# Optimization experiments

Hardware: AMD Instinct MI355X
Metric: run time of the kernel (lower is better)

Reference implementation:

```python
import jax, jax.numpy as jnp
import numpy as np

N_EMBD = 1024
N_HEAD = 16
HEAD_DIM = N_EMBD // N_HEAD
SEQ = 2048
BATCH = 2
WINDOW = 256
SCALE = 1.0 / np.sqrt(HEAD_DIM)
MASK_VALUE = -10000.0


def setup_inputs() -> dict:
    key = jax.random.key(0)
    ks = jax.random.split(key, 5)
    s = 0.02
    return {
        "hidden_states": jax.random.normal(ks[0], (BATCH, SEQ, N_EMBD), dtype=jnp.float32),
        "w_attn": jax.random.normal(ks[1], (N_EMBD, 3 * N_EMBD), dtype=jnp.float32) * s,
        "b_attn": jnp.zeros((3 * N_EMBD,), dtype=jnp.float32),
        "w_proj": jax.random.normal(ks[2], (N_EMBD, N_EMBD), dtype=jnp.float32) * s,
        "b_proj": jnp.zeros((N_EMBD,), dtype=jnp.float32),
    }


def _mask(seq_len):
    # causal AND sliding window: j <= i and j > i - WINDOW
    i = jnp.arange(seq_len)[:, None]
    j = jnp.arange(seq_len)[None, :]
    return (j <= i) & (j > i - WINDOW)  # [T, T] bool


def reference(hidden_states, w_attn, b_attn, w_proj, b_proj):
    B, T, _ = hidden_states.shape
    qkv = hidden_states @ w_attn + b_attn  # [B, T, 3E]
    q, k, v = jnp.split(qkv, 3, axis=-1)
    # [B, H, T, D]
    q = q.reshape(B, T, N_HEAD, HEAD_DIM).transpose(0, 2, 1, 3)
    k = k.reshape(B, T, N_HEAD, HEAD_DIM).transpose(0, 2, 1, 3)
    v = v.reshape(B, T, N_HEAD, HEAD_DIM).transpose(0, 2, 1, 3)

    scores = jnp.einsum("bhqd,bhkd->bhqk", q, k) * SCALE  # [B, H, T, T]
    mask = _mask(T)[None, None]  # [1, 1, T, T]
    scores = jnp.where(mask, scores, MASK_VALUE)
    scores = jnp.clip(scores, -10000.0, 10000.0)
    attn = jax.nn.softmax(scores, axis=-1)
    out = jnp.einsum("bhqk,bhkd->bhqd", attn, v)  # [B, H, T, D]
    out = out.transpose(0, 2, 1, 3).reshape(B, T, N_EMBD)
    return out @ w_proj + b_proj
```

## Files before the change

kernel.cpp:

```cpp
#include <hip/hip_runtime.h>


typedef __bf16 bf16_t;
typedef bf16_t bf16x8 __attribute__((ext_vector_type(8)));
typedef bf16_t bf16x4 __attribute__((ext_vector_type(4)));
typedef float  floatx4 __attribute__((ext_vector_type(4)));

#define SEQ_T   2048
#define NHEAD   16
#define HDIM    64
#define EMB     1024
#define WIN     256
#define SCALE_F 0.125f

__global__ __launch_bounds__(1024) void detect_dtype(
    const uint4* __restrict__ w, int nvec, int* __restrict__ flag)
{
    __shared__ int cnt_s;
    if (threadIdx.x == 0) cnt_s = 0;
    __syncthreads();
    int c = 0;
    for (int i = threadIdx.x; i < nvec; i += 1024) {
        const uint4 v = w[i];
        #pragma unroll
        for (int e = 0; e < 4; ++e) {
            const unsigned int word = (&v.x)[e];
            const unsigned int ex = (word >> 7) & 0xffu;
            c += (ex >= 100u && ex <= 150u) ? 1 : 0;
        }
    }
    #pragma unroll
    for (int m = 32; m >= 1; m >>= 1) c += __shfl_xor(c, m, 64);
    if ((threadIdx.x & 63) == 0) atomicAdd(&cnt_s, c);
    __syncthreads();
    if (threadIdx.x == 0) *flag = (cnt_s * 2 > nvec * 4) ? 1 : 0;
}

__global__ __launch_bounds__(256) void canon_bf16(
    const void* __restrict__ src, bf16_t* __restrict__ dst, int n,
    const int* __restrict__ flag)
{
    const int f = *flag;
    const int i4 = (blockIdx.x * 256 + threadIdx.x) * 4;
    if (i4 >= n) return;
    bf16x4 v;
    if (f) {
        v = *(const bf16x4*)((const bf16_t*)src + i4);
    } else {
        const float4 x = *(const float4*)((const float*)src + i4);
        v[0] = (bf16_t)x.x; v[1] = (bf16_t)x.y;
        v[2] = (bf16_t)x.z; v[3] = (bf16_t)x.w;
    }
    *(bf16x4*)(dst + i4) = v;
}

__global__ __launch_bounds__(256) void transpose_to_bf16(
    const void* __restrict__ W, bf16_t* __restrict__ Wt, int K, int N,
    const int* __restrict__ flag)
{
    __shared__ __align__(16) bf16_t tile[64][68];
    const int f  = *flag;
    const int n0 = blockIdx.x * 64;
    const int k0 = blockIdx.y * 64;
    const int tx = threadIdx.x & 15;
    const int ty = threadIdx.x >> 4;

    #pragma unroll
    for (int r = ty; r < 64; r += 16) {
        bf16x4 v;
        const size_t base = (size_t)(k0 + r) * N + n0 + tx * 4;
        if (f) {
            v = *(const bf16x4*)((const bf16_t*)W + base);
        } else {
            const float4 x = *(const float4*)((const float*)W + base);
            v[0] = (bf16_t)x.x; v[1] = (bf16_t)x.y;
            v[2] = (bf16_t)x.z; v[3] = (bf16_t)x.w;
        }
        *(bf16x4*)&tile[r][tx * 4] = v;
    }
    __syncthreads();
    #pragma unroll
    for (int r = ty; r < 64; r += 16) {
        bf16x4 v;
        v[0] = tile[tx * 4 + 0][r];
        v[1] = tile[tx * 4 + 1][r];
        v[2] = tile[tx * 4 + 2][r];
        v[3] = tile[tx * 4 + 3][r];
        *(bf16x4*)(Wt + (size_t)(n0 + r) * K + k0 + tx * 4) = v;
    }
}

template<int BNt>
__global__ __launch_bounds__(256) void gemm_bt_bias(
    const bf16_t* __restrict__ A,
    const bf16_t* __restrict__ Bt,
    const bf16_t* __restrict__ bias,
    void* __restrict__ C,
    int M, int N, int K,
    int force_bf16, const int* __restrict__ flag)
{
    constexpr int BMt = 128;
    constexpr int NF  = BNt / 32;
    __shared__ __align__(16) bf16_t As[BMt * 64];
    __shared__ __align__(16) bf16_t Bs[BNt * 64];

    const int obf  = force_bf16 | *flag;
    const int tid  = threadIdx.x;
    const int wave = tid >> 6;
    const int lane = tid & 63;
    const int quad = lane >> 4;
    const int n16  = lane & 15;
    const int m0 = blockIdx.y * BMt;
    const int n0 = blockIdx.x * BNt;
    const int wm = (wave >> 1) * 64;
    const int wn = (wave & 1) * (BNt / 2);

    floatx4 acc[4][NF] = {};

    const int lr = lane >> 3;
    const int g8 = ((lane & 7) ^ lr) * 8;

    const int csw = (quad ^ (n16 & 7)) * 8;

    for (int k0 = 0; k0 < K; k0 += 64) {
        #pragma unroll
        for (int t = 0; t < BMt / 32; ++t) {
            const int row0 = wave * (BMt / 4) + t * 8;
            const bf16_t* ga = A + (size_t)(m0 + row0 + lr) * K + k0 + g8;
            __builtin_amdgcn_global_load_lds(
                (const __attribute__((address_space(1))) void*)ga,
                (__attribute__((address_space(3))) void*)(As + row0 * 64),
                16, 0, 0);
        }
        #pragma unroll
        for (int t = 0; t < BNt / 32; ++t) {
            const int row0 = wave * (BNt / 4) + t * 8;
            const bf16_t* gb = Bt + (size_t)(n0 + row0 + lr) * K + k0 + g8;
            __builtin_amdgcn_global_load_lds(
                (const __attribute__((address_space(1))) void*)gb,
                (__attribute__((address_space(3))) void*)(Bs + row0 * 64),
                16, 0, 0);
        }
        __syncthreads();

        #pragma unroll
        for (int s = 0; s < 2; ++s) {
            const int ch = (((4 * s + quad) ^ (n16 & 7)) * 8);
            const bf16_t* pa = As + (wm + n16) * 64 + ch;
            const bf16_t* pb = Bs + (wn + n16) * 64 + ch;
            bf16x8 af[4], bfr[NF];
            #pragma unroll
            for (int ff = 0; ff < 4; ++ff)
                af[ff] = *(const bf16x8*)(pa + ff * 16 * 64);
            #pragma unroll
            for (int ff = 0; ff < NF; ++ff)
                bfr[ff] = *(const bf16x8*)(pb + ff * 16 * 64);
            #pragma unroll
            for (int mf = 0; mf < 4; ++mf)
                #pragma unroll
                for (int nf = 0; nf < NF; ++nf)
                    acc[mf][nf] = __builtin_amdgcn_mfma_f32_16x16x32_bf16(
                        af[mf], bfr[nf], acc[mf][nf], 0, 0, 0);
        }
        __syncthreads();
    }

    const int col   = n0 + wn + n16;
    const int rbase = m0 + wm + quad * 4;
    #pragma unroll
    for (int nf = 0; nf < NF; ++nf) {
        const float bv = (float)bias[col + nf * 16];
        #pragma unroll
        for (int mf = 0; mf < 4; ++mf) {
            #pragma unroll
            for (int r = 0; r < 4; ++r) {
                const size_t idx =
                    (size_t)(rbase + mf * 16 + r) * N + col + nf * 16;
                const float val = acc[mf][nf][r] + bv;
                if (obf) ((bf16_t*)C)[idx] = (bf16_t)val;
                else     ((float*)C)[idx]  = val;
            }
        }
    }
}

#define CW   160
#define VT_S 168
#define P_S  168

__global__ __launch_bounds__(256) void attn_mfma(
    const bf16_t* __restrict__ qkv,
    bf16_t* __restrict__ attn_out)
{
    __shared__ __align__(16) bf16_t Ks[CW * 64];
    __shared__ __align__(16) bf16_t Vt[64 * VT_S];
    __shared__ __align__(16) bf16_t Pst[4][16 * P_S];

    const int tid  = threadIdx.x;
    const int wave = tid >> 6;
    const int lane = tid & 63;
    const int quad = lane >> 4;
    const int n16  = lane & 15;

    const int i0 = blockIdx.x * 64;
    const int h  = blockIdx.y;
    const int b  = blockIdx.z;
    const size_t rowbase = (size_t)b * SEQ_T;
    const int kbase  = i0 - 256;
    const int iw     = 16 * wave;
    const int climit = 256 - i0;

    const bf16_t* Qg = qkv + (rowbase + i0 + iw + n16) * (3 * EMB) + h * HDIM;
    bf16x8 qf[2];
    qf[0] = *(const bf16x8*)(Qg + quad * 8);
    qf[1] = *(const bf16x8*)(Qg + 32 + quad * 8);

    floatx4 Oac[4] = {};
    float m_run[4], l_run[4];
    #pragma unroll
    for (int rr = 0; rr < 4; ++rr) { m_run[rr] = -3.0e38f; l_run[rr] = 0.f; }

    for (int hc = 0; hc < 2; ++hc) {
        const int cbase = hc * CW;

        bf16x8 vreg[5];
        #pragma unroll
        for (int t = 0; t < 5; ++t) {
            const int idx = tid + 256 * t;
            const int lc  = idx >> 3;
            const int d0  = (idx & 7) * 8;
            int j = kbase + cbase + lc; if (j < 0) j = 0;
            vreg[t] = *(const bf16x8*)(qkv + (rowbase + j) * (3 * EMB)
                                       + 2 * EMB + h * HDIM + d0);
        }

        __syncthreads();

        #pragma unroll
        for (int t = 0; t < 5; ++t) {
            const int lc0 = wave * 40 + t * 8;
            const int lcL = lc0 + (lane >> 3);
            int j = kbase + cbase + lcL; if (j < 0) j = 0;
            const int g = (lane & 7) ^ (lcL & 7);
            const bf16_t* src = qkv + (rowbase + j) * (3 * EMB)
                                + EMB + h * HDIM + g * 8;
            __builtin_amdgcn_global_load_lds(
                (const __attribute__((address_space(1))) void*)src,
                (__attribute__((address_space(3))) void*)(Ks + lc0 * 64),
                16, 0, 0);
        }

        #pragma unroll
        for (int t = 0; t < 5; ++t) {
            const int idx = tid + 256 * t;
            const int lc  = idx >> 3;
            const int d0  = (idx & 7) * 8;
            #pragma unroll
            for (int e = 0; e < 8; ++e)
                Vt[(d0 + e) * VT_S + lc] = vreg[t][e];
        }

        __syncthreads();

        floatx4 sc[10];
        #pragma unroll
        for (int tt = 0; tt < 10; ++tt) {
            sc[tt] = (floatx4){0.f, 0.f, 0.f, 0.f};
            #pragma unroll
            for (int s2 = 0; s2 < 2; ++s2) {
                const int lc = 16 * tt + n16;
                const int ch = (4 * s2 + quad) ^ (lc & 7);
                const bf16x8 kf = *(const bf16x8*)(Ks + lc * 64 + ch * 8);
                sc[tt] = __builtin_amdgcn_mfma_f32_16x16x32_bf16(
                    qf[s2], kf, sc[tt], 0, 0, 0);
            }
        }

        #pragma unroll
        for (int tt = 0; tt < 10; ++tt) {
            const int c  = cbase + 16 * tt + n16;
            const int cw = c - iw;
            #pragma unroll
            for (int rr = 0; rr < 4; ++rr) {
                const int r = quad * 4 + rr;
                const bool valid = (cw > r) && (cw <= r + 256) && (c >= climit);
                sc[tt][rr] = valid ? sc[tt][rr] * SCALE_F : -3.0e38f;
            }
        }

        float cm[4];
        #pragma unroll
        for (int rr = 0; rr < 4; ++rr) {
            cm[rr] = -3.0e38f;
            #pragma unroll
            for (int tt = 0; tt < 10; ++tt) cm[rr] = fmaxf(cm[rr], sc[tt][rr]);
            #pragma unroll
            for (int m = 8; m >= 1; m >>= 1)
                cm[rr] = fmaxf(cm[rr], __shfl_xor(cm[rr], m, 64));
        }

        #pragma unroll
        for (int rr = 0; rr < 4; ++rr) {
            const float mnew  = fmaxf(m_run[rr], cm[rr]);
            const float alpha = __expf(m_run[rr] - mnew);
            m_run[rr] = mnew;
            l_run[rr] *= alpha;
            #pragma unroll
            for (int nt = 0; nt < 4; ++nt) Oac[nt][rr] *= alpha;
        }

        float psum[4] = {0.f, 0.f, 0.f, 0.f};
        #pragma unroll
        for (int tt = 0; tt < 10; ++tt) {
            #pragma unroll
            for (int rr = 0; rr < 4; ++rr) {
                const float s = sc[tt][rr];
                const float e = (s > -1.0e38f) ? __expf(s - m_run[rr]) : 0.f;
                psum[rr] += e;
                Pst[wave][(quad * 4 + rr) * P_S + 16 * tt + n16] = (bf16_t)e;
            }
        }
        #pragma unroll
        for (int rr = 0; rr < 4; ++rr) {
            #pragma unroll
            for (int m = 8; m >= 1; m >>= 1)
                psum[rr] += __shfl_xor(psum[rr], m, 64);
            l_run[rr] += psum[rr];
        }

        __syncthreads();

        #pragma unroll
        for (int ks = 0; ks < 5; ++ks) {
            const bf16x8 paf = *(const bf16x8*)(
                &Pst[wave][n16 * P_S + ks * 32 + quad * 8]);
            #pragma unroll
            for (int nt = 0; nt < 4; ++nt) {
                const bf16x8 vbf = *(const bf16x8*)(
                    Vt + (nt * 16 + n16) * VT_S + ks * 32 + quad * 8);
                Oac[nt] = __builtin_amdgcn_mfma_f32_16x16x32_bf16(
                    paf, vbf, Oac[nt], 0, 0, 0);
            }
        }
    }

    #pragma unroll
    for (int rr = 0; rr < 4; ++rr) {
        const float rden = 1.0f / l_run[rr];
        const size_t row = rowbase + i0 + iw + quad * 4 + rr;
        #pragma unroll
        for (int nt = 0; nt < 4; ++nt) {
            attn_out[row * EMB + h * HDIM + nt * 16 + n16] =
                (bf16_t)(Oac[nt][rr] * rden);
        }
    }
}

extern "C" void kernel_launch(void* const* d_in, const int* in_sizes, int n_in,
                              void* d_out, int out_size, void* d_ws, size_t ws_size,
                              hipStream_t stream)
{
    const void* hidden = d_in[0];
    const void* w_attn = d_in[1];
    const void* b_attn = d_in[2];
    const void* w_proj = d_in[3];
    const void* b_proj = d_in[4];

    char* ws = (char*)d_ws;
    bf16_t* Wt_attn = (bf16_t*)(ws);
    bf16_t* Wt_proj = (bf16_t*)(ws + (6u << 20));
    bf16_t* qkv     = (bf16_t*)(ws + (8u << 20));
    bf16_t* attn_o  = (bf16_t*)(ws + (32u << 20));
    bf16_t* Hc      = (bf16_t*)(ws + (40u << 20));
    bf16_t* bb_attn = (bf16_t*)(ws + (48u << 20));
    bf16_t* bb_proj = (bf16_t*)(ws + (48u << 20) + 8192);
    int*    flag    = (int*)   (ws + (48u << 20) + 16384);

    detect_dtype<<<1, 1024, 0, stream>>>((const uint4*)hidden, 4096, flag);

    canon_bf16<<<4096, 256, 0, stream>>>(hidden, Hc, 4096 * 1024, flag);
    canon_bf16<<<3, 256, 0, stream>>>(b_attn, bb_attn, 3072, flag);
    canon_bf16<<<1, 256, 0, stream>>>(b_proj, bb_proj, 1024, flag);

    transpose_to_bf16<<<dim3(3072 / 64, 1024 / 64), 256, 0, stream>>>(
        w_attn, Wt_attn, 1024, 3072, flag);
    transpose_to_bf16<<<dim3(1024 / 64, 1024 / 64), 256, 0, stream>>>(
        w_proj, Wt_proj, 1024, 1024, flag);

    gemm_bt_bias<128><<<dim3(3072 / 128, 4096 / 128), 256, 0, stream>>>(
        Hc, Wt_attn, bb_attn, qkv, 4096, 3072, 1024, 1, flag);

    attn_mfma<<<dim3(SEQ_T / 64, NHEAD, 2), 256, 0, stream>>>(qkv, attn_o);

    gemm_bt_bias<64><<<dim3(1024 / 64, 4096 / 128), 256, 0, stream>>>(
        attn_o, Wt_proj, bb_proj, (void*)d_out, 4096, 1024, 1024, 0, flag);
}
```

Baseline: 190.9 us.

## Fuse preprocessing launches, inline dtype detection, register-staged GEMM prefetch

The separate dtype-detect kernel is replaced by a per-wave inline check of the first 64 vectors of the input. The three canonicalisation launches become one, and the two weight transposes become one, which cuts launch count. When inputs are already bf16 the conversion is skipped and the GEMM reads the raw buffers. The GEMM drops direct global-to-LDS loads in favour of a register-staged prefetch of the next K tile with a swizzled LDS store. This may overlap loads with MFMA work, but it adds register pressure and loses the async LDS load path.

```diff
diff --git a/kernel.cpp b/kernel.cpp
--- a/kernel.cpp
+++ b/kernel.cpp
@@ -13,55 +13,56 @@
 #define WIN     256
 #define SCALE_F 0.125f
 
-__global__ __launch_bounds__(1024) void detect_dtype(
-    const uint4* __restrict__ w, int nvec, int* __restrict__ flag)
-{
-    __shared__ int cnt_s;
-    if (threadIdx.x == 0) cnt_s = 0;
-    __syncthreads();
+__device__ __forceinline__ int detect_bf16(const uint4* __restrict__ det)
+{
+    const int lane = threadIdx.x & 63;
+    const uint4 v = det[lane];
     int c = 0;
-    for (int i = threadIdx.x; i < nvec; i += 1024) {
-        const uint4 v = w[i];
-        #pragma unroll
-        for (int e = 0; e < 4; ++e) {
-            const unsigned int word = (&v.x)[e];
-            const unsigned int ex = (word >> 7) & 0xffu;
-            c += (ex >= 100u && ex <= 150u) ? 1 : 0;
-        }
+    #pragma unroll
+    for (int e = 0; e < 4; ++e) {
+        const unsigned int ex = ((&v.x)[e] >> 7) & 0xffu;
+        c += (ex >= 100u && ex <= 150u) ? 1 : 0;
     }
     #pragma unroll
     for (int m = 32; m >= 1; m >>= 1) c += __shfl_xor(c, m, 64);
-    if ((threadIdx.x & 63) == 0) atomicAdd(&cnt_s, c);
-    __syncthreads();
-    if (threadIdx.x == 0) *flag = (cnt_s * 2 > nvec * 4) ? 1 : 0;
-}
-
-__global__ __launch_bounds__(256) void canon_bf16(
-    const void* __restrict__ src, bf16_t* __restrict__ dst, int n,
-    const int* __restrict__ flag)
-{
-    const int f = *flag;
-    const int i4 = (blockIdx.x * 256 + threadIdx.x) * 4;
-    if (i4 >= n) return;
+    return (c * 2 > 256) ? 1 : 0;
+}
+
+__global__ __launch_bounds__(256) void canon_all(
+    const void* __restrict__ hidden, bf16_t* __restrict__ Hc,
+    const void* __restrict__ ba, bf16_t* __restrict__ bba,
+    const void* __restrict__ bp, bf16_t* __restrict__ bbp)
+{
+    if (detect_bf16((const uint4*)hidden)) return;
+    const int blk = blockIdx.x;
+    const float* src;
+    bf16_t* dst;
+    int base;
+    if (blk < 4096)      { src = (const float*)hidden; dst = Hc;  base = blk * 1024; }
+    else if (blk < 4099) { src = (const float*)ba;     dst = bba; base = (blk - 4096) * 1024; }
+    else                 { src = (const float*)bp;     dst = bbp; base = 0; }
+    const int i4 = base + threadIdx.x * 4;
+    const float4 x = *(const float4*)(src + i4);
     bf16x4 v;
-    if (f) {
-        v = *(const bf16x4*)((const bf16_t*)src + i4);
-    } else {
-        const float4 x = *(const float4*)((const float*)src + i4);
-        v[0] = (bf16_t)x.x; v[1] = (bf16_t)x.y;
-        v[2] = (bf16_t)x.z; v[3] = (bf16_t)x.w;
-    }
+    v[0] = (bf16_t)x.x; v[1] = (bf16_t)x.y;
+    v[2] = (bf16_t)x.z; v[3] = (bf16_t)x.w;
     *(bf16x4*)(dst + i4) = v;
 }
 
-__global__ __launch_bounds__(256) void transpose_to_bf16(
-    const void* __restrict__ W, bf16_t* __restrict__ Wt, int K, int N,
-    const int* __restrict__ flag)
+__global__ __launch_bounds__(256) void transpose_both(
+    const void* __restrict__ wA, bf16_t* __restrict__ WtA,
+    const void* __restrict__ wP, bf16_t* __restrict__ WtP,
+    const uint4* __restrict__ det)
 {
     __shared__ __align__(16) bf16_t tile[64][68];
-    const int f  = *flag;
-    const int n0 = blockIdx.x * 64;
-    const int k0 = blockIdx.y * 64;
+    const int f = detect_bf16(det);
+    int id = blockIdx.x;
+    const void* W; bf16_t* Wt; int N, bx, by;
+    if (id < 768) { W = wA; Wt = WtA; N = 3072; bx = id % 48; by = id / 48; }
+    else { id -= 768; W = wP; Wt = WtP; N = 1024; bx = id % 16; by = id / 16; }
+    const int K = 1024;
+    const int n0 = bx * 64;
+    const int k0 = by * 64;
     const int tx = threadIdx.x & 15;
     const int ty = threadIdx.x >> 4;
 
@@ -92,19 +93,26 @@
 
 template<int BNt>
 __global__ __launch_bounds__(256) void gemm_bt_bias(
-    const bf16_t* __restrict__ A,
+    const bf16_t* __restrict__ Abf,
+    const bf16_t* __restrict__ Aalt,
     const bf16_t* __restrict__ Bt,
-    const bf16_t* __restrict__ bias,
+    const bf16_t* __restrict__ biasbf,
+    const bf16_t* __restrict__ biasalt,
     void* __restrict__ C,
     int M, int N, int K,
-    int force_bf16, const int* __restrict__ flag)
+    int force_bf16, const uint4* __restrict__ det)
 {
     constexpr int BMt = 128;
     constexpr int NF  = BNt / 32;
+    constexpr int NB  = BNt / 32;
     __shared__ __align__(16) bf16_t As[BMt * 64];
     __shared__ __align__(16) bf16_t Bs[BNt * 64];
 
-    const int obf  = force_bf16 | *flag;
+    const int flag = detect_bf16(det);
+    const bf16_t* A    = flag ? Abf    : Aalt;
+    const bf16_t* bias = flag ? biasbf : biasalt;
+    const int obf = force_bf16 | flag;
+
     const int tid  = threadIdx.x;
     const int wave = tid >> 6;
     const int lane = tid & 63;
@@ -117,30 +125,46 @@
 
     floatx4 acc[4][NF] = {};
 
-    const int lr = lane >> 3;
-    const int g8 = ((lane & 7) ^ lr) * 8;
-
-    const int csw = (quad ^ (n16 & 7)) * 8;
+    uint4 rA[4], rB[NB];
+
+    const int arow = tid >> 1;
+    const int acol = (tid & 1) * 32;
+    const int brow = (BNt == 128) ? (tid >> 1) : (tid >> 2);
+    const int bcol = (BNt == 128) ? ((tid & 1) * 32) : ((tid & 3) * 16);
+
+    auto loadA = [&](int kk) {
+        const bf16_t* g = A + (size_t)(m0 + arow) * K + kk + acol;
+        #pragma unroll
+        for (int i = 0; i < 4; ++i) rA[i] = *(const uint4*)(g + i * 8);
+    };
+    auto loadB = [&](int kk) {
+        const bf16_t* g = Bt + (size_t)(n0 + brow) * K + kk + bcol;
+        #pragma unroll
+        for (int i = 0; i < NB; ++i) rB[i] = *(const uint4*)(g + i * 8);
+    };
+    auto storeA = [&]() {
+        #pragma unroll
+        for (int i = 0; i < 4; ++i) {
+            const int g = (acol >> 3) + i;
+            const int s = g ^ (arow & 7);
+            *(uint4*)(As + arow * 64 + s * 8) = rA[i];
+        }
+    };
+    auto storeB = [&]() {
+        #pragma unroll
+        for (int i = 0; i < NB; ++i) {
+            const int g = (bcol >> 3) + i;
+            const int s = g ^ (brow & 7);
+            *(uint4*)(Bs + brow * 64 + s * 8) = rB[i];
+        }
+    };
+
+    loadA(0); loadB(0);
 
     for (int k0 = 0; k0 < K; k0 += 64) {
-        #pragma unroll
-        for (int t = 0; t < BMt / 32; ++t) {
-            const int row0 = wave * (BMt / 4) + t * 8;
-            const bf16_t* ga = A + (size_t)(m0 + row0 + lr) * K + k0 + g8;
-            __builtin_amdgcn_global_load_lds(
-                (const __attribute__((address_space(1))) void*)ga,
-                (__attribute__((address_space(3))) void*)(As + row0 * 64),
-                16, 0, 0);
-        }
-        #pragma unroll
-        for (int t = 0; t < BNt / 32; ++t) {
-            const int row0 = wave * (BNt / 4) + t * 8;
-            const bf16_t* gb = Bt + (size_t)(n0 + row0 + lr) * K + k0 + g8;
-            __builtin_amdgcn_global_load_lds(
-                (const __attribute__((address_space(1))) void*)gb,
-                (__attribute__((address_space(3))) void*)(Bs + row0 * 64),
-                16, 0, 0);
-        }
+        __syncthreads();
+        storeA(); storeB();
+        if (k0 + 64 < K) { loadA(k0 + 64); loadB(k0 + 64); }
         __syncthreads();
 
         #pragma unroll
@@ -162,7 +186,6 @@
                     acc[mf][nf] = __builtin_amdgcn_mfma_f32_16x16x32_bf16(
                         af[mf], bfr[nf], acc[mf][nf], 0, 0, 0);
         }
-        __syncthreads();
     }
 
     const int col   = n0 + wn + n16;
@@ -374,24 +397,22 @@
     bf16_t* Hc      = (bf16_t*)(ws + (40u << 20));
     bf16_t* bb_attn = (bf16_t*)(ws + (48u << 20));
     bf16_t* bb_proj = (bf16_t*)(ws + (48u << 20) + 8192);
-    int*    flag    = (int*)   (ws + (48u << 20) + 16384);
-
-    detect_dtype<<<1, 1024, 0, stream>>>((const uint4*)hidden, 4096, flag);
-
-    canon_bf16<<<4096, 256, 0, stream>>>(hidden, Hc, 4096 * 1024, flag);
-    canon_bf16<<<3, 256, 0, stream>>>(b_attn, bb_attn, 3072, flag);
-    canon_bf16<<<1, 256, 0, stream>>>(b_proj, bb_proj, 1024, flag);
-
-    transpose_to_bf16<<<dim3(3072 / 64, 1024 / 64), 256, 0, stream>>>(
-        w_attn, Wt_attn, 1024, 3072, flag);
-    transpose_to_bf16<<<dim3(1024 / 64, 1024 / 64), 256, 0, stream>>>(
-        w_proj, Wt_proj, 1024, 1024, flag);
+
+    const uint4* det = (const uint4*)hidden;
+
+    canon_all<<<4100, 256, 0, stream>>>(hidden, Hc, b_attn, bb_attn,
+                                        b_proj, bb_proj);
+
+    transpose_both<<<1024, 256, 0, stream>>>(w_attn, Wt_attn,
+                                             w_proj, Wt_proj, det);
 
     gemm_bt_bias<128><<<dim3(3072 / 128, 4096 / 128), 256, 0, stream>>>(
-        Hc, Wt_attn, bb_attn, qkv, 4096, 3072, 1024, 1, flag);
+        (const bf16_t*)hidden, Hc, Wt_attn,
+        (const bf16_t*)b_attn, bb_attn, qkv, 4096, 3072, 1024, 1, det);
 
     attn_mfma<<<dim3(SEQ_T / 64, NHEAD, 2), 256, 0, stream>>>(qkv, attn_o);
 
     gemm_bt_bias<64><<<dim3(1024 / 64, 4096 / 128), 256, 0, stream>>>(
-        attn_o, Wt_proj, bb_proj, (void*)d_out, 4096, 1024, 1024, 0, flag);
-}
+        attn_o, attn_o, Wt_proj,
+        (const bf16_t*)b_proj, bb_proj, (void*)d_out, 4096, 1024, 1024, 0, det);
+}
```

Result: slower. 293.9 us (+54.0%).
